# Kernel optimization log

Measured on AMD Instinct MI355X. Metric: run time of the kernel, lower is better.

The kernel has to match this reference:

```python
import jax, jax.numpy as jnp
import numpy as np
import math

B, S, D, H = 8, 1024, 256, 8
HD = D // H  # head size = 32


def setup_inputs() -> dict:
    key = jax.random.key(0)
    ks = jax.random.split(key, 12)
    inp = {
        "query": jax.random.normal(ks[0], (B, S, D), jnp.float32),
        "key": jax.random.normal(ks[1], (B, S, D), jnp.float32),
        "value": jax.random.normal(ks[2], (B, S, D), jnp.float32),
        "rel": jax.random.uniform(ks[3], (B, S, S), jnp.float32),
        "timestamp": jax.random.normal(ks[4], (B, S, S), jnp.float32),
        "l1": jax.random.uniform(ks[5], (1,), jnp.float32),
        "l2": jax.random.uniform(ks[6], (1,), jnp.float32),
        # projection weights (nn.Linear: y = x @ W.T + b)
        "Wq": jax.random.normal(ks[7], (D, D), jnp.float32) / math.sqrt(D),
        "bq": jnp.zeros((D,), jnp.float32),
        "Wk": jax.random.normal(ks[8], (D, D), jnp.float32) / math.sqrt(D),
        "bk": jnp.zeros((D,), jnp.float32),
        "Wv": jax.random.normal(ks[9], (D, D), jnp.float32) / math.sqrt(D),
        "bv": jnp.zeros((D,), jnp.float32),
    }
    return inp


def reference(query, key, value, rel, timestamp, l1, l2, Wq, bq, Wk, bk, Wv, bv):
    b, s, d = query.shape
    h, hd = H, HD

    def proj(x, W, bias):
        # [b,s,d] -> [b,h,s,hd]
        return (x @ W.T + bias).reshape(b, s, h, hd).transpose(0, 2, 1, 3)

    q = proj(query, Wq, bq)
    k = proj(key, Wk, bk)
    v = proj(value, Wv, bv)

    # causal future mask: True above the diagonal (future positions)
    mask = jnp.triu(jnp.ones((s, s), dtype=bool), k=1)[None, None]  # [1,1,s,s]

    # relation attention: rel * mask, zeros -> -10000, softmax
    relm = rel[:, None] * mask.astype(rel.dtype)  # broadcast over heads [b,1->h,s,s]
    rel_attn = jax.nn.softmax(jnp.where(relm == 0, jnp.float32(-10000.0), relm), axis=-1)

    # scaled dot-product scores with causal mask
    scores = jnp.einsum('bhqd,bhkd->bhqk', q, k) / math.sqrt(hd)
    scores = jnp.where(mask, jnp.float32(-1e9), scores)
    prob_attn = jax.nn.softmax(scores, axis=-1)

    # time-decay attention: exp(-|t|), masked to -inf (use -1e30 for grad safety)
    ts = jnp.where(mask, jnp.float32(-1e30), jnp.exp(-jnp.abs(timestamp[:, None])))
    time_attn = jax.nn.softmax(ts, axis=-1)

    # blend (time_include=True, qrelation_include=True)
    prob = (1.0 - l2) * prob_attn + l2 * time_attn
    prob = (1.0 - l1) * prob + l1 * rel_attn

    out = jnp.einsum('bhqk,bhkd->bhqd', prob, v)
    out = out.transpose(0, 2, 1, 3).reshape(b, s, d)
    return out
```

## Files before the change

### kernel.cpp

```cpp
#include <hip/hip_runtime.h>
#include <math.h>

constexpr int B = 8, S = 1024, D = 256, H = 8, HD = 32;

typedef __attribute__((ext_vector_type(8))) short bf16x8;
typedef __attribute__((ext_vector_type(16))) float f32x16;
typedef __attribute__((ext_vector_type(2)))  int  int2v;

__device__ __forceinline__ uint cvtpk(float a, float b) {
    uint r;
    asm("v_cvt_pk_bf16_f32 %0, %1, %2" : "=v"(r) : "v"(a), "v"(b));
    return r;
}
__device__ __forceinline__ float xswap32f(float v, int hi) {
    int2v t = __builtin_amdgcn_permlane32_swap(__float_as_int(v), __float_as_int(v), false, false);
    return __int_as_float(hi ? t[0] : t[1]);
}

__global__ __launch_bounds__(512, 4) void proj_mfma(
    const float* __restrict__ query, const float* __restrict__ key_,
    const float* __restrict__ value,
    const float* __restrict__ Wq, const float* __restrict__ Wk,
    const float* __restrict__ Wv,
    const float* __restrict__ bq, const float* __restrict__ bk,
    const float* __restrict__ bv, float qscale,
    ushort* __restrict__ qbuf, ushort* __restrict__ kbuf,
    ushort* __restrict__ vtbuf, float* __restrict__ cpart)
{
    __shared__ ushort xf[8192];
    __shared__ float bias_lds[256];

    const int m = blockIdx.y;
    const int tid = threadIdx.x;
    const int w = tid >> 6, lane = tid & 63;
    const int l31 = lane & 31, hi = lane >> 5;
    const int h = w;

    const float* xsrc = (m == 0) ? query : (m == 1) ? key_ : value;
    const float* Wsrc = (m == 0) ? Wq : (m == 1) ? Wk : Wv;
    const float* bsrc = (m == 0) ? bq : (m == 1) ? bk : bv;
    ushort* yb = (m == 0) ? qbuf : (m == 1) ? kbuf : vtbuf;
    const float wscale = (m == 0) ? qscale : 1.0f;

    if (tid < 256) bias_lds[tid] = bsrc[tid] * wscale;

    bf16x8 wf[16];
    {
        const float* wrow = Wsrc + ((size_t)(h * 32 + l31)) * 256 + hi * 8;
        #pragma unroll
        for (int kc = 0; kc < 16; ++kc) {
            float4 a = *(const float4*)(wrow + kc * 16);
            float4 b = *(const float4*)(wrow + kc * 16 + 4);
            uint4 p;
            p.x = cvtpk(a.x * wscale, a.y * wscale);
            p.y = cvtpk(a.z * wscale, a.w * wscale);
            p.z = cvtpk(b.x * wscale, b.y * wscale);
            p.w = cvtpk(b.z * wscale, b.w * wscale);
            wf[kc] = __builtin_bit_cast(bf16x8, p);
        }
    }

    const int sst = tid & 31, skc = tid >> 5;
    float cpacc = 0.f;

    for (int it = 0; it < 2; ++it) {
        const int stile = blockIdx.x * 2 + it;
        const int b_ = stile >> 5, t32 = stile & 31;

        __syncthreads();
        {
            const float* xrow = xsrc + ((size_t)(stile * 32 + sst)) * 256 + skc * 16;
            float4 a0 = *(const float4*)(xrow + 0);
            float4 a1 = *(const float4*)(xrow + 4);
            float4 a2 = *(const float4*)(xrow + 8);
            float4 a3 = *(const float4*)(xrow + 12);
            uint2 w01 = { cvtpk(a0.x, a0.y), cvtpk(a0.z, a0.w) };
            uint2 w23 = { cvtpk(a1.x, a1.y), cvtpk(a1.z, a1.w) };
            uint2 w45 = { cvtpk(a2.x, a2.y), cvtpk(a2.z, a2.w) };
            uint2 w67 = { cvtpk(a3.x, a3.y), cvtpk(a3.z, a3.w) };
            ushort* base = xf + skc * 512 + sst * 4;
            *(uint2*)(base +   0) = w01;
            *(uint2*)(base + 128) = w23;
            *(uint2*)(base + 256) = w45;
            *(uint2*)(base + 384) = w67;
        }
        __syncthreads();

        f32x16 acc;
        #pragma unroll
        for (int r = 0; r < 16; ++r) acc[r] = 0.f;
        #pragma unroll
        for (int kc = 0; kc < 16; ++kc) {
            const ushort* rb = xf + kc * 512 + hi * 256 + l31 * 4;
            uint2 lo = *(const uint2*)rb;
            uint2 hj = *(const uint2*)(rb + 128);
            uint4 xw = { lo.x, lo.y, hj.x, hj.y };
            bf16x8 xfrag = __builtin_bit_cast(bf16x8, xw);
            if (m < 2)
                acc = __builtin_amdgcn_mfma_f32_32x32x16_bf16(wf[kc], xfrag, acc, 0, 0, 0);
            else
                acc = __builtin_amdgcn_mfma_f32_32x32x16_bf16(xfrag, wf[kc], acc, 0, 0, 0);
        }

        if (m < 2) {
            #pragma unroll
            for (int r = 0; r < 16; ++r)
                acc[r] += bias_lds[h * 32 + (r & 3) + 8 * (r >> 2) + 4 * hi];
        } else {
            const float bl = bias_lds[h * 32 + l31];
            #pragma unroll
            for (int r = 0; r < 16; ++r) acc[r] += bl;
            float cp = 0.f;
            #pragma unroll
            for (int r = 0; r < 16; ++r) cp += acc[r];
            cp += __shfl_xor(cp, 32);
            cpacc += cp;
        }

        uint wa0 = cvtpk(acc[0], acc[1]),   wa1 = cvtpk(acc[2], acc[3]);
        uint wb0 = cvtpk(acc[4], acc[5]),   wb1 = cvtpk(acc[6], acc[7]);
        uint wa2 = cvtpk(acc[8], acc[9]),   wa3 = cvtpk(acc[10], acc[11]);
        uint wb2 = cvtpk(acc[12], acc[13]), wb3 = cvtpk(acc[14], acc[15]);
        int2v s0 = __builtin_amdgcn_permlane32_swap((int)wa0, (int)wb0, false, false);
        int2v s1 = __builtin_amdgcn_permlane32_swap((int)wa1, (int)wb1, false, false);
        int2v s2 = __builtin_amdgcn_permlane32_swap((int)wa2, (int)wb2, false, false);
        int2v s3 = __builtin_amdgcn_permlane32_swap((int)wa3, (int)wb3, false, false);
        uint4 p0 = { (uint)s0[0], (uint)s1[0], (uint)s0[1], (uint)s1[1] };
        uint4 p1 = { (uint)s2[0], (uint)s3[0], (uint)s2[1], (uint)s3[1] };
        ushort* dst = yb + (((size_t)b_ * H + h) * 32 + t32) * 1024 + hi * 256 + l31 * 8;
        *(uint4*)dst = p0;
        *(uint4*)(dst + 512) = p1;
    }
    if (m == 2 && hi == 0)
        cpart[blockIdx.x * D + h * 32 + l31] = cpacc;
}

__global__ __launch_bounds__(512, 4) void timerel_mfma(
    const float* __restrict__ ts, const float* __restrict__ rel,
    const ushort* __restrict__ vtb, const float* __restrict__ cpart,
    const float* __restrict__ l1p, const float* __restrict__ l2p,
    float* __restrict__ out)
{
    __shared__ ushort wlds[64 * 512];
    __shared__ float rsum[2][8][32];
    __shared__ float normt[32], normr[32], nuni[32];

    const int b  = blockIdx.y;
    const int i0 = blockIdx.x * 32;
    const int w = threadIdx.x >> 6, lane = threadIdx.x & 63;
    const int l31 = lane & 31, hi = lane >> 5;
    const int hi8 = hi * 8;
    const int i = i0 + l31;

    const float* tsrow  = ts  + ((size_t)b * S + i) * S + hi8;
    const float* relrow = rel + ((size_t)b * S + i) * S + hi8;

    float wreg[8][8];
    float st = 0.f, sr = 0.f;
    const int ks0 = w * 8;
    #pragma unroll
    for (int kk = 0; kk < 8; ++kk) {
        const int ks = ks0 + kk;
        const int js = ks * 16;
        const bool allPast = (js + 15 <= i0);
        const bool allFut  = (js >= i0 + 32);
        if (allPast) {
            float tv[8];
            *(float4*)&tv[0] = *(const float4*)(tsrow + js);
            *(float4*)&tv[4] = *(const float4*)(tsrow + js + 4);
            #pragma unroll
            for (int q = 0; q < 8; ++q) {
                float v = __expf(__expf(-fabsf(tv[q])));
                st += v; wreg[kk][q] = v;
            }
        } else if (allFut) {
            float rv[8];
            *(float4*)&rv[0] = *(const float4*)(relrow + js);
            *(float4*)&rv[4] = *(const float4*)(relrow + js + 4);
            #pragma unroll
            for (int q = 0; q < 8; ++q) {
                float v = (rv[q] != 0.f) ? __expf(rv[q]) : 0.f;
                sr += v; wreg[kk][q] = v;
            }
        } else {
            float tv[8], rv[8];
            *(float4*)&tv[0] = *(const float4*)(tsrow + js);
            *(float4*)&tv[4] = *(const float4*)(tsrow + js + 4);
            *(float4*)&rv[0] = *(const float4*)(relrow + js);
            *(float4*)&rv[4] = *(const float4*)(relrow + js + 4);
            #pragma unroll
            for (int q = 0; q < 8; ++q) {
                const int j = js + hi8 + q;
                float v;
                if (j <= i) { v = __expf(__expf(-fabsf(tv[q]))); st += v; }
                else        { v = (rv[q] != 0.f) ? __expf(rv[q]) : 0.f; sr += v; }
                wreg[kk][q] = v;
            }
        }
    }

    st += __shfl_xor(st, 32);
    sr += __shfl_xor(sr, 32);
    if (hi == 0) { rsum[0][w][l31] = st; rsum[1][w][l31] = sr; }
    __syncthreads();

    if (threadIdx.x < 32) {
        const int r = threadIdx.x;
        float stt = 0.f, srt = 0.f;
        #pragma unroll
        for (int q = 0; q < 8; ++q) { stt += rsum[0][q][r]; srt += rsum[1][q][r]; }
        const float l1 = l1p[0], l2 = l2p[0];
        normt[r] = (1.f - l1) * l2 / stt;
        normr[r] = (srt > 0.5f) ? (l1 / srt) : 0.f;
        nuni[r]  = (srt > 0.5f) ? 0.f : (l1 / (float)S);
    }
    __syncthreads();

    {
        const float nt = normt[l31], nr = normr[l31];
        #pragma unroll
        for (int kk = 0; kk < 8; ++kk) {
            const int ks = ks0 + kk;
            const int js = ks * 16;
            uint wp[4];
            #pragma unroll
            for (int q = 0; q < 4; ++q) {
                const int j0 = js + hi8 + 2 * q;
                float a = wreg[kk][2 * q]     * ((j0     <= i) ? nt : nr);
                float c = wreg[kk][2 * q + 1] * ((j0 + 1 <= i) ? nt : nr);
                wp[q] = cvtpk(a, c);
            }
            ushort* base = wlds + ks * 512 + hi * 256 + l31 * 4;
            uint2 v0; v0.x = wp[0]; v0.y = wp[1];
            uint2 v1; v1.x = wp[2]; v1.y = wp[3];
            *(uint2*)(base)       = v0;
            *(uint2*)(base + 128) = v1;
        }
    }
    __syncthreads();

    const ushort* vtbase = vtb + ((size_t)b * 8 + w) * 32768 + hi * 256 + l31 * 8;
    f32x16 acc;
    #pragma unroll
    for (int r = 0; r < 16; ++r) acc[r] = 0.f;
    #pragma unroll 4
    for (int ks = 0; ks < 64; ++ks) {
        const ushort* rb = wlds + ks * 512 + hi * 256 + l31 * 4;
        uint2 lo = *(const uint2*)rb;
        uint2 hj = *(const uint2*)(rb + 128);
        uint4 aw = { lo.x, lo.y, hj.x, hj.y };
        bf16x8 afrag = __builtin_bit_cast(bf16x8, aw);
        bf16x8 vf = *(const bf16x8*)(vtbase + (size_t)ks * 512);
        acc = __builtin_amdgcn_mfma_f32_32x32x16_bf16(afrag, vf, acc, 0, 0, 0);
    }

    const int d = w * 32 + l31;
    float cv = 0.f;
    if (i0 == S - 32) {
        #pragma unroll
        for (int p_ = 0; p_ < 16; ++p_)
            cv += cpart[(b * 16 + p_) * D + d];
    }
    float* obase = out + ((size_t)b * S + i0) * D + d;
    #pragma unroll
    for (int r = 0; r < 16; ++r) {
        const int row = (r & 3) + 8 * (r >> 2) + 4 * hi;
        obase[(size_t)row * D] = acc[r] + nuni[row] * cv;
    }
}

#define LOADKV(K0, K1, V0, V1, KT) do { \
    const ushort* kp_ = kbase + (size_t)(KT) * 1024; \
    const ushort* vp_ = vbase + (size_t)(KT) * 1024; \
    K0 = *(const bf16x8*)kp_;        K1 = *(const bf16x8*)(kp_ + 512); \
    V0 = *(const bf16x8*)vp_;        V1 = *(const bf16x8*)(vp_ + 512); \
} while (0)

#define TILE_COMPUTE(K0, K1, V0, V1, ISDIAG) do { \
    f32x16 stv; \
    _Pragma("unroll") for (int r = 0; r < 16; ++r) stv[r] = 0.f; \
    stv = __builtin_amdgcn_mfma_f32_32x32x16_bf16(K0, qf0, stv, 0, 0, 0); \
    stv = __builtin_amdgcn_mfma_f32_32x32x16_bf16(K1, qf1, stv, 0, 0, 0); \
    if (ISDIAG) { \
        _Pragma("unroll") for (int r = 0; r < 16; ++r) \
            if (((r & 3) + 8 * (r >> 2) + 4 * hi) > l31) stv[r] = -1e30f; \
    } \
    float p[16]; \
    _Pragma("unroll") for (int r = 0; r < 16; ++r) { p[r] = exp2f(stv[r]); lacc += p[r]; } \
    uint wa0 = cvtpk(p[0], p[1]),   wa1 = cvtpk(p[2], p[3]); \
    uint wb0 = cvtpk(p[4], p[5]),   wb1 = cvtpk(p[6], p[7]); \
    uint wa2 = cvtpk(p[8], p[9]),   wa3 = cvtpk(p[10], p[11]); \
    uint wb2 = cvtpk(p[12], p[13]), wb3 = cvtpk(p[14], p[15]); \
    int2v s0 = __builtin_amdgcn_permlane32_swap((int)wa0, (int)wb0, false, false); \
    int2v s1 = __builtin_amdgcn_permlane32_swap((int)wa1, (int)wb1, false, false); \
    int2v s2 = __builtin_amdgcn_permlane32_swap((int)wa2, (int)wb2, false, false); \
    int2v s3 = __builtin_amdgcn_permlane32_swap((int)wa3, (int)wb3, false, false); \
    uint4 pa0i = { (uint)s0[0], (uint)s1[0], (uint)s0[1], (uint)s1[1] }; \
    uint4 pa1i = { (uint)s2[0], (uint)s3[0], (uint)s2[1], (uint)s3[1] }; \
    bf16x8 pa0 = __builtin_bit_cast(bf16x8, pa0i); \
    bf16x8 pa1 = __builtin_bit_cast(bf16x8, pa1i); \
    ot = __builtin_amdgcn_mfma_f32_32x32x16_bf16(V0, pa0, ot, 0, 0, 0); \
    ot = __builtin_amdgcn_mfma_f32_32x32x16_bf16(V1, pa1, ot, 0, 0, 0); \
} while (0)

__global__ __launch_bounds__(512, 4) void flash_mfma(
    const ushort* __restrict__ qb, const ushort* __restrict__ kb,
    const ushort* __restrict__ vtb, const float* __restrict__ l1p,
    const float* __restrict__ l2p, float* __restrict__ out)
{
    __shared__ float mbuf[4][64][18];
    __shared__ float lds_t[4][32 * 33];
    const int id = blockIdx.x;
    const int halfg = id >> 8, rr_ = id & 255;
    const int qraw = rr_ >> 5;
    const int qblk = halfg ? (7 - qraw) : qraw;
    const int bh = (rr_ & 31) | (halfg << 5);
    const int b = bh >> 3, h = bh & 7;
    const int w = threadIdx.x >> 6, lane = threadIdx.x & 63;
    const int sub = w & 3, half = w >> 2;
    const int l31 = lane & 31, hi = lane >> 5;
    const int qt = qblk * 4 + sub;
    const float c_p = (1.f - l1p[0]) * (1.f - l2p[0]);

    const ushort* qp_ = qb + ((size_t)bh * 32 + qt) * 1024 + hi * 256 + l31 * 8;
    const bf16x8 qf0 = *(const bf16x8*)qp_;
    const bf16x8 qf1 = *(const bf16x8*)(qp_ + 512);
    const ushort* kbase = kb  + (size_t)bh * 32768 + hi * 256 + l31 * 8;
    const ushort* vbase = vtb + (size_t)bh * 32768 + hi * 256 + l31 * 8;

    f32x16 ot;
    #pragma unroll
    for (int r = 0; r < 16; ++r) ot[r] = 0.f;
    float lacc = 0.f;

    const int nlo = (qt + 1) >> 1;
    const int klo = half ? nlo : 0;
    const int khi = half ? qt : (nlo - 1);

    if (klo <= khi) {
        bf16x8 kA0, kA1, vA0, vA1, kB0, kB1, vB0, vB1;
        LOADKV(kA0, kA1, vA0, vA1, klo);
        int kt = klo;
        for (;;) {
            if (kt + 1 <= khi) LOADKV(kB0, kB1, vB0, vB1, kt + 1);
            TILE_COMPUTE(kA0, kA1, vA0, vA1, kt == qt);
            if (++kt > khi) break;
            if (kt + 1 <= khi) LOADKV(kA0, kA1, vA0, vA1, kt + 1);
            TILE_COMPUTE(kB0, kB1, vB0, vB1, kt == qt);
            if (++kt > khi) break;
        }
    }

    if (half == 1) {
        float* mb = &mbuf[sub][lane][0];
        #pragma unroll
        for (int r = 0; r < 16; r += 4)
            *(float4*)&mb[r] = make_float4(ot[r], ot[r+1], ot[r+2], ot[r+3]);
        mb[16] = lacc;
    }
    __syncthreads();

    if (half == 0) {
        const float* mb = &mbuf[sub][lane][0];
        #pragma unroll
        for (int r = 0; r < 16; ++r) ot[r] += mb[r];
        lacc += mb[16];
        const float lrun = lacc + xswap32f(lacc, hi);
        const float inv = c_p / lrun;
        float* lt = lds_t[sub];
        #pragma unroll
        for (int r = 0; r < 16; ++r) {
            const int d = (r & 3) + 8 * (r >> 2) + 4 * hi;
            lt[l31 * 33 + d] = ot[r] * inv;
        }
    }
    __syncthreads();
    if (half == 0) {
        const int q0w = qt * 32;
        const float* lt = lds_t[sub];
        #pragma unroll
        for (int rr = 0; rr < 4; ++rr) {
            const int ql = rr * 8 + (lane >> 3);
            const int d0 = (lane & 7) * 4;
            const float* lp = &lt[ql * 33 + d0];
            float* op = out + ((size_t)b * S + q0w + ql) * D + h * 32 + d0;
            float4 cur = *(const float4*)op;
            cur.x += lp[0]; cur.y += lp[1]; cur.z += lp[2]; cur.w += lp[3];
            *(float4*)op = cur;
        }
    }
}

extern "C" void kernel_launch(void* const* d_in, const int* in_sizes, int n_in,
                              void* d_out, int out_size, void* d_ws, size_t ws_size,
                              hipStream_t stream)
{
    (void)in_sizes; (void)n_in; (void)out_size; (void)ws_size;
    const float* query = (const float*)d_in[0];
    const float* key_  = (const float*)d_in[1];
    const float* value = (const float*)d_in[2];
    const float* rel   = (const float*)d_in[3];
    const float* tsp   = (const float*)d_in[4];
    const float* l1p   = (const float*)d_in[5];
    const float* l2p   = (const float*)d_in[6];
    const float* Wq    = (const float*)d_in[7];
    const float* bq    = (const float*)d_in[8];
    const float* Wk    = (const float*)d_in[9];
    const float* bk    = (const float*)d_in[10];
    const float* Wv    = (const float*)d_in[11];
    const float* bv    = (const float*)d_in[12];
    float* out = (float*)d_out;

    ushort* qbuf  = (ushort*)d_ws;
    ushort* kbuf  = (ushort*)((char*)d_ws + (4u  << 20));
    ushort* vtbuf = (ushort*)((char*)d_ws + (8u  << 20));
    float*  cpart = (float*)((char*)d_ws + (12u << 20));

    const float qscale = 1.4426950408889634f * 0.17677669529663687f;

    proj_mfma<<<dim3(128, 3), 512, 0, stream>>>(
        query, key_, value, Wq, Wk, Wv, bq, bk, bv, qscale,
        qbuf, kbuf, vtbuf, cpart);

    timerel_mfma<<<dim3(S / 32, B), 512, 0, stream>>>(
        tsp, rel, vtbuf, cpart, l1p, l2p, out);

    flash_mfma<<<512, 512, 0, stream>>>(qbuf, kbuf, vtbuf, l1p, l2p, out);
}
```

Before: 61.95 us.

## Assign rows to waves in timerel and use padded row-major weight LDS

Each wave now handles four full rows of the ts/rel matrices with fully coalesced float4 loads across the row. Row sums come from a wave-wide shuffle reduction, which removes the cross-wave LDS reduction and one block barrier. Weights are stored row-major in a padded LDS array, so the MFMA A-fragment becomes a single 16-byte LDS read. The costs are more shuffle instructions, a serial loop over rows, and a possible change in LDS bank conflicts.

```diff
diff --git a/kernel.cpp b/kernel.cpp
--- a/kernel.cpp
+++ b/kernel.cpp
@@ -141,100 +141,73 @@
     const float* __restrict__ l1p, const float* __restrict__ l2p,
     float* __restrict__ out)
 {
-    __shared__ ushort wlds[64 * 512];
-    __shared__ float rsum[2][8][32];
-    __shared__ float normt[32], normr[32], nuni[32];
+    __shared__ ushort wlds[32][1032];
+    __shared__ float nuni[32];
 
     const int b  = blockIdx.y;
     const int i0 = blockIdx.x * 32;
     const int w = threadIdx.x >> 6, lane = threadIdx.x & 63;
     const int l31 = lane & 31, hi = lane >> 5;
-    const int hi8 = hi * 8;
-    const int i = i0 + l31;
-
-    const float* tsrow  = ts  + ((size_t)b * S + i) * S + hi8;
-    const float* relrow = rel + ((size_t)b * S + i) * S + hi8;
-
-    float wreg[8][8];
-    float st = 0.f, sr = 0.f;
-    const int ks0 = w * 8;
-    #pragma unroll
-    for (int kk = 0; kk < 8; ++kk) {
-        const int ks = ks0 + kk;
-        const int js = ks * 16;
-        const bool allPast = (js + 15 <= i0);
-        const bool allFut  = (js >= i0 + 32);
-        if (allPast) {
-            float tv[8];
-            *(float4*)&tv[0] = *(const float4*)(tsrow + js);
-            *(float4*)&tv[4] = *(const float4*)(tsrow + js + 4);
-            #pragma unroll
-            for (int q = 0; q < 8; ++q) {
-                float v = __expf(__expf(-fabsf(tv[q])));
-                st += v; wreg[kk][q] = v;
+    const float l1 = l1p[0], l2 = l2p[0];
+
+    for (int r = 0; r < 4; ++r) {
+        const int row = w * 4 + r;
+        const int i = i0 + row;
+        const float* tsrow  = ts  + ((size_t)b * S + i) * S;
+        const float* relrow = rel + ((size_t)b * S + i) * S;
+
+        float wv[4][4];
+        float stp = 0.f, srp = 0.f;
+        #pragma unroll
+        for (int q = 0; q < 4; ++q) {
+            const int jb = q * 256 + lane * 4;
+            if (q * 256 + 255 <= i) {
+                float4 t4 = *(const float4*)(tsrow + jb);
+                const float te[4] = { t4.x, t4.y, t4.z, t4.w };
+                #pragma unroll
+                for (int e = 0; e < 4; ++e) {
+                    float v = __expf(__expf(-fabsf(te[e])));
+                    stp += v; wv[q][e] = v;
+                }
+            } else if (q * 256 > i) {
+                float4 r4 = *(const float4*)(relrow + jb);
+                const float re[4] = { r4.x, r4.y, r4.z, r4.w };
+                #pragma unroll
+                for (int e = 0; e < 4; ++e) {
+                    float v = (re[e] != 0.f) ? __expf(re[e]) : 0.f;
+                    srp += v; wv[q][e] = v;
+                }
+            } else {
+                float4 t4 = *(const float4*)(tsrow + jb);
+                float4 r4 = *(const float4*)(relrow + jb);
+                const float te[4] = { t4.x, t4.y, t4.z, t4.w };
+                const float re[4] = { r4.x, r4.y, r4.z, r4.w };
+                #pragma unroll
+                for (int e = 0; e < 4; ++e) {
+                    float v;
+                    if (jb + e <= i) { v = __expf(__expf(-fabsf(te[e]))); stp += v; }
+                    else             { v = (re[e] != 0.f) ? __expf(re[e]) : 0.f; srp += v; }
+                    wv[q][e] = v;
+                }
             }
-        } else if (allFut) {
-            float rv[8];
-            *(float4*)&rv[0] = *(const float4*)(relrow + js);
-            *(float4*)&rv[4] = *(const float4*)(relrow + js + 4);
-            #pragma unroll
-            for (int q = 0; q < 8; ++q) {
-                float v = (rv[q] != 0.f) ? __expf(rv[q]) : 0.f;
-                sr += v; wreg[kk][q] = v;
-            }
-        } else {
-            float tv[8], rv[8];
-            *(float4*)&tv[0] = *(const float4*)(tsrow + js);
-            *(float4*)&tv[4] = *(const float4*)(tsrow + js + 4);
-            *(float4*)&rv[0] = *(const float4*)(relrow + js);
-            *(float4*)&rv[4] = *(const float4*)(relrow + js + 4);
-            #pragma unroll
-            for (int q = 0; q < 8; ++q) {
-                const int j = js + hi8 + q;
-                float v;
-                if (j <= i) { v = __expf(__expf(-fabsf(tv[q]))); st += v; }
-                else        { v = (rv[q] != 0.f) ? __expf(rv[q]) : 0.f; sr += v; }
-                wreg[kk][q] = v;
-            }
-        }
-    }
-
-    st += __shfl_xor(st, 32);
-    sr += __shfl_xor(sr, 32);
-    if (hi == 0) { rsum[0][w][l31] = st; rsum[1][w][l31] = sr; }
-    __syncthreads();
-
-    if (threadIdx.x < 32) {
-        const int r = threadIdx.x;
-        float stt = 0.f, srt = 0.f;
-        #pragma unroll
-        for (int q = 0; q < 8; ++q) { stt += rsum[0][q][r]; srt += rsum[1][q][r]; }
-        const float l1 = l1p[0], l2 = l2p[0];
-        normt[r] = (1.f - l1) * l2 / stt;
-        normr[r] = (srt > 0.5f) ? (l1 / srt) : 0.f;
-        nuni[r]  = (srt > 0.5f) ? 0.f : (l1 / (float)S);
-    }
-    __syncthreads();
-
-    {
-        const float nt = normt[l31], nr = normr[l31];
-        #pragma unroll
-        for (int kk = 0; kk < 8; ++kk) {
-            const int ks = ks0 + kk;
-            const int js = ks * 16;
-            uint wp[4];
-            #pragma unroll
-            for (int q = 0; q < 4; ++q) {
-                const int j0 = js + hi8 + 2 * q;
-                float a = wreg[kk][2 * q]     * ((j0     <= i) ? nt : nr);
-                float c = wreg[kk][2 * q + 1] * ((j0 + 1 <= i) ? nt : nr);
-                wp[q] = cvtpk(a, c);
-            }
-            ushort* base = wlds + ks * 512 + hi * 256 + l31 * 4;
-            uint2 v0; v0.x = wp[0]; v0.y = wp[1];
-            uint2 v1; v1.x = wp[2]; v1.y = wp[3];
-            *(uint2*)(base)       = v0;
-            *(uint2*)(base + 128) = v1;
+        }
+        #pragma unroll
+        for (int off = 1; off < 64; off <<= 1) {
+            stp += __shfl_xor(stp, off);
+            srp += __shfl_xor(srp, off);
+        }
+        const float nt = (1.f - l1) * l2 / stp;
+        const float nr = (srp > 0.5f) ? (l1 / srp) : 0.f;
+        if (lane == 0) nuni[row] = (srp > 0.5f) ? 0.f : (l1 / (float)S);
+        #pragma unroll
+        for (int q = 0; q < 4; ++q) {
+            const int jb = q * 256 + lane * 4;
+            float a0 = wv[q][0] * ((jb     <= i) ? nt : nr);
+            float a1 = wv[q][1] * ((jb + 1 <= i) ? nt : nr);
+            float a2 = wv[q][2] * ((jb + 2 <= i) ? nt : nr);
+            float a3 = wv[q][3] * ((jb + 3 <= i) ? nt : nr);
+            uint2 pk; pk.x = cvtpk(a0, a1); pk.y = cvtpk(a2, a3);
+            *(uint2*)&wlds[row][jb] = pk;
         }
     }
     __syncthreads();
@@ -245,11 +218,7 @@
     for (int r = 0; r < 16; ++r) acc[r] = 0.f;
     #pragma unroll 4
     for (int ks = 0; ks < 64; ++ks) {
-        const ushort* rb = wlds + ks * 512 + hi * 256 + l31 * 4;
-        uint2 lo = *(const uint2*)rb;
-        uint2 hj = *(const uint2*)(rb + 128);
-        uint4 aw = { lo.x, lo.y, hj.x, hj.y };
-        bf16x8 afrag = __builtin_bit_cast(bf16x8, aw);
+        bf16x8 afrag = *(const bf16x8*)&wlds[l31][ks * 16 + hi * 8];
         bf16x8 vf = *(const bf16x8*)(vtbase + (size_t)ks * 512);
         acc = __builtin_amdgcn_mfma_f32_32x32x16_bf16(afrag, vf, acc, 0, 0, 0);
     }
```

Result: slower. 66.44 us (+7.2%).

## Defer row normalization past MFMA by splitting time/rel accumulators

Applied to the files above, without the earlier changes.

The timerel kernel now writes unnormalized bf16 weights straight to LDS during the load phase. It keeps separate time and relation accumulators and applies the per-row normalizers only at output. This drops the 64-float wreg register array, the second rescale pass and one barrier. Two extra LDS slots hold the relation half of the diagonal tiles, which adds two MFMA steps. Launch bounds occupancy drops from 4 to 2, and bf16 rounding now happens before normalization.

```diff
diff --git a/kernel.cpp b/kernel.cpp
--- a/kernel.cpp
+++ b/kernel.cpp
@@ -135,18 +135,19 @@
         cpart[blockIdx.x * D + h * 32 + l31] = cpacc;
 }
 
-__global__ __launch_bounds__(512, 4) void timerel_mfma(
+__global__ __launch_bounds__(512, 2) void timerel_mfma(
     const float* __restrict__ ts, const float* __restrict__ rel,
     const ushort* __restrict__ vtb, const float* __restrict__ cpart,
     const float* __restrict__ l1p, const float* __restrict__ l2p,
     float* __restrict__ out)
 {
-    __shared__ ushort wlds[64 * 512];
+    __shared__ ushort wlds[66 * 512];
     __shared__ float rsum[2][8][32];
     __shared__ float normt[32], normr[32], nuni[32];
 
     const int b  = blockIdx.y;
     const int i0 = blockIdx.x * 32;
+    const int ksd = i0 >> 4;
     const int w = threadIdx.x >> 6, lane = threadIdx.x & 63;
     const int l31 = lane & 31, hi = lane >> 5;
     const int hi8 = hi * 8;
@@ -155,47 +156,76 @@
     const float* tsrow  = ts  + ((size_t)b * S + i) * S + hi8;
     const float* relrow = rel + ((size_t)b * S + i) * S + hi8;
 
-    float wreg[8][8];
     float st = 0.f, sr = 0.f;
     const int ks0 = w * 8;
     #pragma unroll
     for (int kk = 0; kk < 8; ++kk) {
         const int ks = ks0 + kk;
         const int js = ks * 16;
-        const bool allPast = (js + 15 <= i0);
-        const bool allFut  = (js >= i0 + 32);
-        if (allPast) {
+        ushort* slotT = wlds + ks * 512 + hi * 256 + l31 * 4;
+        if (ks < ksd) {
             float tv[8];
             *(float4*)&tv[0] = *(const float4*)(tsrow + js);
             *(float4*)&tv[4] = *(const float4*)(tsrow + js + 4);
-            #pragma unroll
-            for (int q = 0; q < 8; ++q) {
-                float v = __expf(__expf(-fabsf(tv[q])));
-                st += v; wreg[kk][q] = v;
+            uint wp[4];
+            #pragma unroll
+            for (int q = 0; q < 4; ++q) {
+                float w0 = __expf(__expf(-fabsf(tv[2 * q])));
+                float w1 = __expf(__expf(-fabsf(tv[2 * q + 1])));
+                st += w0 + w1;
+                wp[q] = cvtpk(w0, w1);
             }
-        } else if (allFut) {
+            uint2 v0; v0.x = wp[0]; v0.y = wp[1];
+            uint2 v1; v1.x = wp[2]; v1.y = wp[3];
+            *(uint2*)slotT         = v0;
+            *(uint2*)(slotT + 128) = v1;
+        } else if (ks > ksd + 1) {
             float rv[8];
             *(float4*)&rv[0] = *(const float4*)(relrow + js);
             *(float4*)&rv[4] = *(const float4*)(relrow + js + 4);
-            #pragma unroll
-            for (int q = 0; q < 8; ++q) {
-                float v = (rv[q] != 0.f) ? __expf(rv[q]) : 0.f;
-                sr += v; wreg[kk][q] = v;
+            uint wp[4];
+            #pragma unroll
+            for (int q = 0; q < 4; ++q) {
+                float r0 = rv[2 * q], r1 = rv[2 * q + 1];
+                float w0 = (r0 != 0.f) ? __expf(r0) : 0.f;
+                float w1 = (r1 != 0.f) ? __expf(r1) : 0.f;
+                sr += w0 + w1;
+                wp[q] = cvtpk(w0, w1);
             }
+            uint2 v0; v0.x = wp[0]; v0.y = wp[1];
+            uint2 v1; v1.x = wp[2]; v1.y = wp[3];
+            *(uint2*)slotT         = v0;
+            *(uint2*)(slotT + 128) = v1;
         } else {
             float tv[8], rv[8];
             *(float4*)&tv[0] = *(const float4*)(tsrow + js);
             *(float4*)&tv[4] = *(const float4*)(tsrow + js + 4);
             *(float4*)&rv[0] = *(const float4*)(relrow + js);
             *(float4*)&rv[4] = *(const float4*)(relrow + js + 4);
-            #pragma unroll
-            for (int q = 0; q < 8; ++q) {
-                const int j = js + hi8 + q;
-                float v;
-                if (j <= i) { v = __expf(__expf(-fabsf(tv[q]))); st += v; }
-                else        { v = (rv[q] != 0.f) ? __expf(rv[q]) : 0.f; sr += v; }
-                wreg[kk][q] = v;
+            uint wpT[4], wpR[4];
+            #pragma unroll
+            for (int q = 0; q < 4; ++q) {
+                const int j0 = js + hi8 + 2 * q;
+                const bool p0 = (j0     <= i), p1 = (j0 + 1 <= i);
+                float t0 = __expf(__expf(-fabsf(tv[2 * q])));
+                float t1 = __expf(__expf(-fabsf(tv[2 * q + 1])));
+                float r0 = (rv[2 * q]     != 0.f) ? __expf(rv[2 * q])     : 0.f;
+                float r1 = (rv[2 * q + 1] != 0.f) ? __expf(rv[2 * q + 1]) : 0.f;
+                float wT0 = p0 ? t0 : 0.f, wT1 = p1 ? t1 : 0.f;
+                float wR0 = p0 ? 0.f : r0, wR1 = p1 ? 0.f : r1;
+                st += wT0 + wT1; sr += wR0 + wR1;
+                wpT[q] = cvtpk(wT0, wT1);
+                wpR[q] = cvtpk(wR0, wR1);
             }
+            uint2 t0v; t0v.x = wpT[0]; t0v.y = wpT[1];
+            uint2 t1v; t1v.x = wpT[2]; t1v.y = wpT[3];
+            *(uint2*)slotT         = t0v;
+            *(uint2*)(slotT + 128) = t1v;
+            ushort* slotR = wlds + (64 + (ks - ksd)) * 512 + hi * 256 + l31 * 4;
+            uint2 r0v; r0v.x = wpR[0]; r0v.y = wpR[1];
+            uint2 r1v; r1v.x = wpR[2]; r1v.y = wpR[3];
+            *(uint2*)slotR         = r0v;
+            *(uint2*)(slotR + 128) = r1v;
         }
     }
 
@@ -216,43 +246,29 @@
     }
     __syncthreads();
 
-    {
-        const float nt = normt[l31], nr = normr[l31];
-        #pragma unroll
-        for (int kk = 0; kk < 8; ++kk) {
-            const int ks = ks0 + kk;
-            const int js = ks * 16;
-            uint wp[4];
-            #pragma unroll
-            for (int q = 0; q < 4; ++q) {
-                const int j0 = js + hi8 + 2 * q;
-                float a = wreg[kk][2 * q]     * ((j0     <= i) ? nt : nr);
-                float c = wreg[kk][2 * q + 1] * ((j0 + 1 <= i) ? nt : nr);
-                wp[q] = cvtpk(a, c);
-            }
-            ushort* base = wlds + ks * 512 + hi * 256 + l31 * 4;
-            uint2 v0; v0.x = wp[0]; v0.y = wp[1];
-            uint2 v1; v1.x = wp[2]; v1.y = wp[3];
-            *(uint2*)(base)       = v0;
-            *(uint2*)(base + 128) = v1;
-        }
-    }
-    __syncthreads();
-
     const ushort* vtbase = vtb + ((size_t)b * 8 + w) * 32768 + hi * 256 + l31 * 8;
-    f32x16 acc;
+    f32x16 accT, accR;
     #pragma unroll
-    for (int r = 0; r < 16; ++r) acc[r] = 0.f;
+    for (int r = 0; r < 16; ++r) { accT[r] = 0.f; accR[r] = 0.f; }
+
+    #define MSTEP(SLOT, VCH, ACC) do { \
+        const ushort* rb = wlds + (SLOT) * 512 + hi * 256 + l31 * 4; \
+        uint2 lo = *(const uint2*)rb; \
+        uint2 hj = *(const uint2*)(rb + 128); \
+        uint4 aw = { lo.x, lo.y, hj.x, hj.y }; \
+        bf16x8 afrag = __builtin_bit_cast(bf16x8, aw); \
+        bf16x8 vf = *(const bf16x8*)(vtbase + (size_t)(VCH) * 512); \
+        ACC = __builtin_amdgcn_mfma_f32_32x32x16_bf16(afrag, vf, ACC, 0, 0, 0); \
+    } while (0)
+
+    const int nT = ksd + 2;
     #pragma unroll 4
-    for (int ks = 0; ks < 64; ++ks) {
-        const ushort* rb = wlds + ks * 512 + hi * 256 + l31 * 4;
-        uint2 lo = *(const uint2*)rb;
-        uint2 hj = *(const uint2*)(rb + 128);
-        uint4 aw = { lo.x, lo.y, hj.x, hj.y };
-        bf16x8 afrag = __builtin_bit_cast(bf16x8, aw);
-        bf16x8 vf = *(const bf16x8*)(vtbase + (size_t)ks * 512);
-        acc = __builtin_amdgcn_mfma_f32_32x32x16_bf16(afrag, vf, acc, 0, 0, 0);
-    }
+    for (int ks = 0; ks < nT; ++ks) MSTEP(ks, ks, accT);
+    MSTEP(64, ksd,     accR);
+    MSTEP(65, ksd + 1, accR);
+    #pragma unroll 4
+    for (int ks = nT; ks < 64; ++ks) MSTEP(ks, ks, accR);
+    #undef MSTEP
 
     const int d = w * 32 + l31;
     float cv = 0.f;
@@ -265,7 +281,8 @@
     #pragma unroll
     for (int r = 0; r < 16; ++r) {
         const int row = (r & 3) + 8 * (r >> 2) + 4 * hi;
-        obase[(size_t)row * D] = acc[r] + nuni[row] * cv;
+        obase[(size_t)row * D] =
+            accT[r] * normt[row] + accR[r] * normr[row] + nuni[row] * cv;
     }
 }
 
```

New measurement: 65.00 us. +4.9%, slower.
